# Performance work log

Hardware: AMD Instinct MI355X
Metric: run time of the kernel (lower is better)

Reference implementation:

```python
import jax, jax.numpy as jnp
import numpy as np

ALPHA = 1.0

def setup_inputs() -> dict:
    key = jax.random.key(0)
    X = jax.random.normal(key, (8192, 64), dtype=jnp.float32)
    return {"X": X}

def reference(X) -> jnp.ndarray:
    # Pairwise squared L2 distances via GEMM trick: ||x_i||^2 + ||x_j||^2 - 2 x_i.x_j
    sq = jnp.sum(X * X, axis=1)                      # [N]
    d2 = sq[:, None] + sq[None, :] - 2.0 * (X @ X.T)  # [N, N]
    d2 = jnp.maximum(d2, 0.0)
    # sigma^2 = alpha * mean(d2), detached (no grad through bandwidth)
    sigma_sq = ALPHA * jax.lax.stop_gradient(jnp.mean(d2))
    return jnp.exp(-d2 / (2.0 * sigma_sq))
```

## Files before the change

### kernel.cpp

```cpp
#include <hip/hip_runtime.h>
#include <hip/hip_bf16.h>

#define N 8192
#define D 64

typedef __attribute__((ext_vector_type(8))) short bf16x8;
typedef __attribute__((ext_vector_type(4))) float f32x4;

__device__ inline unsigned short f2b(float f) {
    __hip_bfloat16 h = __float2bfloat16(f);
    return __builtin_bit_cast(unsigned short, h);
}

__global__ __launch_bounds__(256) void gk_prep(const float4* __restrict__ X4,
                                               ushort4* __restrict__ Xb4,
                                               float* __restrict__ sq) {
    const int g = blockIdx.x * 256 + threadIdx.x;
    float4 v = X4[g];
    ushort4 b;
    b.x = f2b(v.x); b.y = f2b(v.y); b.z = f2b(v.z); b.w = f2b(v.w);
    Xb4[g] = b;
    float ss = v.x * v.x + v.y * v.y + v.z * v.z + v.w * v.w;
    ss += __shfl_xor(ss, 8, 16);
    ss += __shfl_xor(ss, 4, 16);
    ss += __shfl_xor(ss, 2, 16);
    ss += __shfl_xor(ss, 1, 16);
    if ((threadIdx.x & 15) == 0) sq[g >> 4] = ss;
}

__global__ __launch_bounds__(256) void gk_colsum(const float* __restrict__ X,
                                                 float* __restrict__ V) {
    __shared__ float red[256];
    const int c = blockIdx.x;
    float s = 0.f;
    for (int r = threadIdx.x; r < N; r += 256) s += X[r * D + c];
    red[threadIdx.x] = s;
    __syncthreads();
    for (int off = 128; off > 0; off >>= 1) {
        if (threadIdx.x < off) red[threadIdx.x] += red[threadIdx.x + off];
        __syncthreads();
    }
    if (threadIdx.x == 0) V[c] = red[0];
}

__global__ __launch_bounds__(256) void gk_finalize(const float* __restrict__ sq,
                                                   const float* __restrict__ V,
                                                   float* __restrict__ scal) {
    __shared__ float red[256];
    float s = 0.f;
    for (int r = threadIdx.x; r < N; r += 256) s += sq[r];
    red[threadIdx.x] = s;
    __syncthreads();
    for (int off = 128; off > 0; off >>= 1) {
        if (threadIdx.x < off) red[threadIdx.x] += red[threadIdx.x + off];
        __syncthreads();
    }
    const float S = red[0];
    __syncthreads();
    float v = (threadIdx.x < D) ? V[threadIdx.x] : 0.f;
    red[threadIdx.x] = v * v;
    __syncthreads();
    for (int off = 128; off > 0; off >>= 1) {
        if (threadIdx.x < off) red[threadIdx.x] += red[threadIdx.x + off];
        __syncthreads();
    }
    if (threadIdx.x == 0) {
        const float Vsq = red[0];
        const float fN = (float)N;
        const float mean = 2.f * S / fN - 2.f * Vsq / (fN * fN);
        const float sigma_sq = 1.0f * mean;
        scal[0] = 1.f / (2.f * sigma_sq);
    }
}

__global__ __launch_bounds__(256) void gk_main(const unsigned short* __restrict__ Xb,
                                               const float* __restrict__ sq,
                                               const float* __restrict__ scal,
                                               float* __restrict__ out) {
    const int lane = threadIdx.x & 63;
    const int wave = threadIdx.x >> 6;
    const int i0 = blockIdx.x * 64 + wave * 16;
    const int j0 = blockIdx.y * 128;
    const int m = lane & 15;
    const int q = lane >> 4;
    const float c0 = scal[0];

    const bf16x8* Arow = reinterpret_cast<const bf16x8*>(Xb + (i0 + m) * D + 8 * q);
    const bf16x8 a0 = Arow[0];
    const bf16x8 a1 = Arow[4];

    f32x4 acc[8];
#pragma unroll
    for (int t = 0; t < 8; ++t) acc[t] = (f32x4){0.f, 0.f, 0.f, 0.f};

#pragma unroll
    for (int t = 0; t < 8; ++t) {
        const bf16x8* Brow =
            reinterpret_cast<const bf16x8*>(Xb + (j0 + t * 16 + m) * D + 8 * q);
        const bf16x8 b0 = Brow[0];
        const bf16x8 b1 = Brow[4];
        acc[t] = __builtin_amdgcn_mfma_f32_16x16x32_bf16(a0, b0, acc[t], 0, 0, 0);
        acc[t] = __builtin_amdgcn_mfma_f32_16x16x32_bf16(a1, b1, acc[t], 0, 0, 0);
    }

    float sqi[4];
#pragma unroll
    for (int r = 0; r < 4; ++r) sqi[r] = sq[i0 + 4 * q + r];

#pragma unroll
    for (int t = 0; t < 8; ++t) {
        const int col = j0 + t * 16 + m;
        const float sqj = sq[col];
#pragma unroll
        for (int r = 0; r < 4; ++r) {
            float d2 = sqi[r] + sqj - 2.0f * acc[t][r];
            d2 = fmaxf(d2, 0.0f);
            out[(size_t)(i0 + 4 * q + r) * N + col] = __expf(-d2 * c0);
        }
    }
}

extern "C" void kernel_launch(void* const* d_in, const int* in_sizes, int n_in,
                              void* d_out, int out_size, void* d_ws, size_t ws_size,
                              hipStream_t stream) {
    const float* X = (const float*)d_in[0];
    float* out = (float*)d_out;

    char* ws = (char*)d_ws;
    unsigned short* Xb = (unsigned short*)ws;
    float* sq = (float*)(ws + 1048576);
    float* V  = (float*)(ws + 1048576 + 32768);
    float* scal = (float*)(ws + 1048576 + 32768 + 256);

    gk_prep<<<512, 256, 0, stream>>>((const float4*)X, (ushort4*)Xb, sq);
    gk_colsum<<<D, 256, 0, stream>>>(X, V);
    gk_finalize<<<1, 256, 0, stream>>>(sq, V, scal);

    dim3 grid(N / 64, N / 128);
    gk_main<<<grid, 256, 0, stream>>>(Xb, sq, scal, out);
}
```

Measured before the change: 315.6 us.

## Fuse column-sum into prep kernel and transpose MFMA output for vectorized nontemporal stores

Column sums are now computed as per-block partial sums inside the prep kernel and reduced in finalize, which removes the separate strided colsum kernel and one launch. The main kernel swaps the A and B operands so each lane holds four consecutive output columns of one row. The 256 MB output is then written with 16-byte nontemporal vector stores instead of scattered scalar stores. The grid is also reordered so that blockIdx.x walks the columns. Finalize now has to read 512x64 partial sums, which adds a small amount of serial work on a single block.

New measurement: 351.1 us. 1.11x slower.

```diff
diff --git a/kernel.cpp b/kernel.cpp
--- a/kernel.cpp
+++ b/kernel.cpp
@@ -14,8 +14,11 @@
 
 __global__ __launch_bounds__(256) void gk_prep(const float4* __restrict__ X4,
                                                ushort4* __restrict__ Xb4,
-                                               float* __restrict__ sq) {
-    const int g = blockIdx.x * 256 + threadIdx.x;
+                                               float* __restrict__ sq,
+                                               float4* __restrict__ Vp4) {
+    __shared__ float4 sm[256];
+    const int tid = threadIdx.x;
+    const int g = blockIdx.x * 256 + tid;
     float4 v = X4[g];
     ushort4 b;
     b.x = f2b(v.x); b.y = f2b(v.y); b.z = f2b(v.z); b.w = f2b(v.w);
@@ -25,51 +28,59 @@
     ss += __shfl_xor(ss, 4, 16);
     ss += __shfl_xor(ss, 2, 16);
     ss += __shfl_xor(ss, 1, 16);
-    if ((threadIdx.x & 15) == 0) sq[g >> 4] = ss;
-}
-
-__global__ __launch_bounds__(256) void gk_colsum(const float* __restrict__ X,
-                                                 float* __restrict__ V) {
-    __shared__ float red[256];
-    const int c = blockIdx.x;
-    float s = 0.f;
-    for (int r = threadIdx.x; r < N; r += 256) s += X[r * D + c];
-    red[threadIdx.x] = s;
+    if ((tid & 15) == 0) sq[g >> 4] = ss;
+    sm[tid] = v;
     __syncthreads();
-    for (int off = 128; off > 0; off >>= 1) {
-        if (threadIdx.x < off) red[threadIdx.x] += red[threadIdx.x + off];
+#pragma unroll
+    for (int off = 128; off >= 16; off >>= 1) {
+        if (tid < off) {
+            float4 o = sm[tid + off];
+            float4 m = sm[tid];
+            m.x += o.x; m.y += o.y; m.z += o.z; m.w += o.w;
+            sm[tid] = m;
+        }
         __syncthreads();
     }
-    if (threadIdx.x == 0) V[c] = red[0];
+    if (tid < 16) Vp4[blockIdx.x * 16 + tid] = sm[tid];
 }
 
 __global__ __launch_bounds__(256) void gk_finalize(const float* __restrict__ sq,
-                                                   const float* __restrict__ V,
+                                                   const float* __restrict__ Vp,
                                                    float* __restrict__ scal) {
     __shared__ float red[256];
+    const int tid = threadIdx.x;
     float s = 0.f;
-    for (int r = threadIdx.x; r < N; r += 256) s += sq[r];
-    red[threadIdx.x] = s;
+    for (int r = tid; r < N; r += 256) s += sq[r];
+    red[tid] = s;
     __syncthreads();
     for (int off = 128; off > 0; off >>= 1) {
-        if (threadIdx.x < off) red[threadIdx.x] += red[threadIdx.x + off];
+        if (tid < off) red[tid] += red[tid + off];
         __syncthreads();
     }
     const float S = red[0];
     __syncthreads();
-    float v = (threadIdx.x < D) ? V[threadIdx.x] : 0.f;
-    red[threadIdx.x] = v * v;
+    const int c = tid & 63, p = tid >> 6;
+    float v = 0.f;
+    for (int r = p; r < 512; r += 4) v += Vp[r * 64 + c];
+    red[tid] = v;
+    __syncthreads();
+    if (tid < 128) red[tid] += red[tid + 128];
+    __syncthreads();
+    if (tid < 64) red[tid] += red[tid + 64];
+    __syncthreads();
+    float vv = (tid < 64) ? red[tid] * red[tid] : 0.f;
+    __syncthreads();
+    red[tid] = vv;
     __syncthreads();
     for (int off = 128; off > 0; off >>= 1) {
-        if (threadIdx.x < off) red[threadIdx.x] += red[threadIdx.x + off];
+        if (tid < off) red[tid] += red[tid + off];
         __syncthreads();
     }
-    if (threadIdx.x == 0) {
+    if (tid == 0) {
         const float Vsq = red[0];
         const float fN = (float)N;
         const float mean = 2.f * S / fN - 2.f * Vsq / (fN * fN);
-        const float sigma_sq = 1.0f * mean;
-        scal[0] = 1.f / (2.f * sigma_sq);
+        scal[0] = 1.f / (2.f * mean);
     }
 }
 
@@ -79,15 +90,15 @@
                                                float* __restrict__ out) {
     const int lane = threadIdx.x & 63;
     const int wave = threadIdx.x >> 6;
-    const int i0 = blockIdx.x * 64 + wave * 16;
-    const int j0 = blockIdx.y * 128;
+    const int i0 = blockIdx.y * 64 + wave * 16;
+    const int j0 = blockIdx.x * 128;
     const int m = lane & 15;
     const int q = lane >> 4;
     const float c0 = scal[0];
 
-    const bf16x8* Arow = reinterpret_cast<const bf16x8*>(Xb + (i0 + m) * D + 8 * q);
-    const bf16x8 a0 = Arow[0];
-    const bf16x8 a1 = Arow[4];
+    const bf16x8* Brow = reinterpret_cast<const bf16x8*>(Xb + (i0 + m) * D + 8 * q);
+    const bf16x8 b0 = Brow[0];
+    const bf16x8 b1 = Brow[4];
 
     f32x4 acc[8];
 #pragma unroll
@@ -95,28 +106,25 @@
 
 #pragma unroll
     for (int t = 0; t < 8; ++t) {
-        const bf16x8* Brow =
+        const bf16x8* Arow =
             reinterpret_cast<const bf16x8*>(Xb + (j0 + t * 16 + m) * D + 8 * q);
-        const bf16x8 b0 = Brow[0];
-        const bf16x8 b1 = Brow[4];
-        acc[t] = __builtin_amdgcn_mfma_f32_16x16x32_bf16(a0, b0, acc[t], 0, 0, 0);
-        acc[t] = __builtin_amdgcn_mfma_f32_16x16x32_bf16(a1, b1, acc[t], 0, 0, 0);
+        acc[t] = __builtin_amdgcn_mfma_f32_16x16x32_bf16(Arow[0], b0, acc[t], 0, 0, 0);
+        acc[t] = __builtin_amdgcn_mfma_f32_16x16x32_bf16(Arow[4], b1, acc[t], 0, 0, 0);
     }
 
-    float sqi[4];
-#pragma unroll
-    for (int r = 0; r < 4; ++r) sqi[r] = sq[i0 + 4 * q + r];
+    const float sqi = sq[i0 + m];
+    float* orow = out + (size_t)(i0 + m) * N + j0 + 4 * q;
+    const f32x4* sq4 = reinterpret_cast<const f32x4*>(sq + j0 + 4 * q);
 
 #pragma unroll
     for (int t = 0; t < 8; ++t) {
-        const int col = j0 + t * 16 + m;
-        const float sqj = sq[col];
-#pragma unroll
-        for (int r = 0; r < 4; ++r) {
-            float d2 = sqi[r] + sqj - 2.0f * acc[t][r];
-            d2 = fmaxf(d2, 0.0f);
-            out[(size_t)(i0 + 4 * q + r) * N + col] = __expf(-d2 * c0);
-        }
+        const f32x4 sj = sq4[t * 4];
+        f32x4 e;
+        e[0] = __expf(-fmaxf(sqi + sj[0] - 2.f * acc[t][0], 0.f) * c0);
+        e[1] = __expf(-fmaxf(sqi + sj[1] - 2.f * acc[t][1], 0.f) * c0);
+        e[2] = __expf(-fmaxf(sqi + sj[2] - 2.f * acc[t][2], 0.f) * c0);
+        e[3] = __expf(-fmaxf(sqi + sj[3] - 2.f * acc[t][3], 0.f) * c0);
+        __builtin_nontemporal_store(e, reinterpret_cast<f32x4*>(orow + t * 16));
     }
 }
 
@@ -128,14 +136,13 @@
 
     char* ws = (char*)d_ws;
     unsigned short* Xb = (unsigned short*)ws;
-    float* sq = (float*)(ws + 1048576);
-    float* V  = (float*)(ws + 1048576 + 32768);
-    float* scal = (float*)(ws + 1048576 + 32768 + 256);
+    float* sq = (float*)(ws + (1 << 20));
+    float* Vp = (float*)(ws + (1 << 20) + (32 << 10));
+    float* scal = (float*)(ws + (1 << 20) + (32 << 10) + (128 << 10));
 
-    gk_prep<<<512, 256, 0, stream>>>((const float4*)X, (ushort4*)Xb, sq);
-    gk_colsum<<<D, 256, 0, stream>>>(X, V);
-    gk_finalize<<<1, 256, 0, stream>>>(sq, V, scal);
+    gk_prep<<<512, 256, 0, stream>>>((const float4*)X, (ushort4*)Xb, sq, (float4*)Vp);
+    gk_finalize<<<1, 256, 0, stream>>>(sq, Vp, scal);
 
-    dim3 grid(N / 64, N / 128);
+    dim3 grid(N / 128, N / 64);
     gk_main<<<grid, 256, 0, stream>>>(Xb, sq, scal, out);
 }
```
